# Kernel tuning notes

Hardware: AMD Instinct MI355X
Metric: run time of the kernel (lower is better)

Reference implementation:

```python
import jax, jax.numpy as jnp
import numpy as np

# ROIAlign config (torchvision semantics, aligned=False)
SPATIAL_SCALE = 0.25
POOLED = 7
SAMPLING_RATIO = 2
MODE = "max"  # from __init__ mode='max'


def setup_inputs() -> dict:
    key = jax.random.key(0)
    kf, kcx, kcy, kw, kh, kb = jax.random.split(key, 6)
    B, C, H, W = 2, 256, 200, 304
    N = 512
    IMG_H, IMG_W = H / SPATIAL_SCALE, W / SPATIAL_SCALE
    feature = jax.random.normal(kf, (B, C, H, W), dtype=jnp.float32)
    cx = jax.random.uniform(kcx, (N,)) * IMG_W
    cy = jax.random.uniform(kcy, (N,)) * IMG_H
    bw = jax.random.uniform(kw, (N,)) * 192.0 + 16.0
    bh = jax.random.uniform(kh, (N,)) * 192.0 + 16.0
    x1 = jnp.clip(cx - bw * 0.5, 0.0, IMG_W - 2.0)
    y1 = jnp.clip(cy - bh * 0.5, 0.0, IMG_H - 2.0)
    x2 = jnp.clip(cx + bw * 0.5, x1 + 1.0, IMG_W - 1.0)
    y2 = jnp.clip(cy + bh * 0.5, y1 + 1.0, IMG_H - 1.0)
    boxes = jnp.stack([x1, y1, x2, y2], axis=1).astype(jnp.float32)
    batch_idx = jax.random.randint(kb, (N,), 0, B, dtype=jnp.int32)
    return {"feature": feature, "boxes": boxes, "batch_idx": batch_idx}


def _sample_coords(start, size):
    # start,size: [N]; returns [N, POOLED*SAMPLING_RATIO] sample coordinates
    bin_sz = size / POOLED                         # [N]
    p = jnp.arange(POOLED, dtype=jnp.float32)      # bin index
    s = (jnp.arange(SAMPLING_RATIO, dtype=jnp.float32) + 0.5) / SAMPLING_RATIO
    # coord = start + (p + s) * bin_sz  -> [N, POOLED, RATIO]
    c = start[:, None, None] + (p[None, :, None] + s[None, None, :]) * bin_sz[:, None, None]
    return c.reshape(c.shape[0], POOLED * SAMPLING_RATIO)


def roi_align(feature, boxes, batch_idx):
    B, C, H, W = feature.shape
    roi = boxes * SPATIAL_SCALE                    # [N,4] in feature coords
    rs_x, rs_y, re_x, re_y = roi[:, 0], roi[:, 1], roi[:, 2], roi[:, 3]
    roi_w = jnp.maximum(re_x - rs_x, 1.0)
    roi_h = jnp.maximum(re_y - rs_y, 1.0)
    ys = _sample_coords(rs_y, roi_h)               # [N, Sy]
    xs = _sample_coords(rs_x, roi_w)               # [N, Sx]
    y = jnp.broadcast_to(ys[:, :, None], (ys.shape[0], ys.shape[1], xs.shape[1]))
    x = jnp.broadcast_to(xs[:, None, :], y.shape)  # [N, Sy, Sx]

    valid = (y > -1.0) & (y < H) & (x > -1.0) & (x < W)
    y = jnp.clip(y, 0.0, H - 1)
    x = jnp.clip(x, 0.0, W - 1)
    y0 = jnp.floor(y).astype(jnp.int32)
    x0 = jnp.floor(x).astype(jnp.int32)
    y1 = jnp.minimum(y0 + 1, H - 1)
    x1 = jnp.minimum(x0 + 1, W - 1)
    ly = y - y0.astype(y.dtype)
    lx = x - x0.astype(x.dtype)
    hy, hx = 1.0 - ly, 1.0 - lx
    b = batch_idx[:, None, None]
    # advanced indexing -> [N, Sy, Sx, C]
    val = (hy * hx)[..., None] * feature[b, :, y0, x0] \
        + (hy * lx)[..., None] * feature[b, :, y0, x1] \
        + (ly * hx)[..., None] * feature[b, :, y1, x0] \
        + (ly * lx)[..., None] * feature[b, :, y1, x1]
    val = jnp.where(valid[..., None], val, 0.0)
    N = boxes.shape[0]
    val = val.reshape(N, POOLED, SAMPLING_RATIO, POOLED, SAMPLING_RATIO, C)
    if MODE == "max":
        out = val.max(axis=(2, 4))                 # [N, PH, PW, C]
    else:
        out = val.mean(axis=(2, 4))
    return jnp.transpose(out, (0, 3, 1, 2))        # [N, C, PH, PW]


def reference(feature, boxes, batch_idx):
    return roi_align(feature, boxes, batch_idx)
```

## Files before the change

### kernel.cpp

```cpp
#include <hip/hip_runtime.h>


#define SS 0.25f
#define POOLED 7

constexpr int Cc = 256;
constexpr int Hc = 200;
constexpr int Wc = 304;
constexpr int Nc = 512;

constexpr int CELLS   = 49;
constexpr int PER_BOX = Cc * CELLS;
constexpr int PLANE   = Hc * Wc;
constexpr int NSAMP   = 14;
constexpr int TILES   = Cc / 4;
constexpr int DEPTH   = 5;
constexpr int GRPF    = 260;
constexpr int BUF_A   = 4 * GRPF;
constexpr int BUF_B   = 3 * GRPF;
constexpr int WAVE_A  = DEPTH * BUF_A;
constexpr int WAVE_B  = DEPTH * BUF_B;
constexpr int CH_F    = WAVE_A + WAVE_B;
constexpr int LDS_F   = 4 * CH_F;
constexpr size_t WS_NEED = (size_t)Nc * sizeof(int);

__global__ __launch_bounds__(64) void box_rank_kernel(
    const float* __restrict__ boxes,
    const int*   __restrict__ batch_idx,
    int*         __restrict__ perm)
{
    const int n = blockIdx.x;
    const int l = threadIdx.x;

    const float cyn  = (boxes[n * 4 + 1] + boxes[n * 4 + 3]) * (0.5f * SS);
    const int  bandn = min(3, max(0, (int)(cyn * (4.0f / (float)Hc))));
    const int  keyn  = batch_idx[n] * 4 + bandn;

    int rank = 0;
    #pragma unroll
    for (int m = 0; m < Nc / 64; ++m) {
        const int j = m * 64 + l;
        const float cyj  = (boxes[j * 4 + 1] + boxes[j * 4 + 3]) * (0.5f * SS);
        const int  bandj = min(3, max(0, (int)(cyj * (4.0f / (float)Hc))));
        const int  keyj  = batch_idx[j] * 4 + bandj;
        const bool lt = (keyj < keyn) || (keyj == keyn && j < n);
        rank += (int)__popcll(__ballot(lt));
    }
    if (l == 0) perm[rank] = n;
}

template <bool USE_PERM>
__global__ __launch_bounds__(512) void roi_align_max_kernel(
    const float* __restrict__ feature,
    const float* __restrict__ boxes,
    const int*   __restrict__ batch_idx,
    const int*   __restrict__ perm,
    float*       __restrict__ out)
{
    __shared__ float lds[LDS_F];

    const int bid = blockIdx.x;
    const int n = USE_PERM ? perm[(bid & 7) * 64 + (bid >> 3)] : bid;
    const int tid  = threadIdx.x;
    const int wv   = tid >> 6;
    const int lane = tid & 63;
    const int chl  = wv >> 1;
    const int role = wv & 1;
    const int NI    = role ? 3 : 4;
    const int BUF   = role ? BUF_B : BUF_A;
    const int wbase = chl * CH_F + (role ? WAVE_A : 0);
    const int HALF  = role ? 6 : 8;
    const int SYB   = role ? 8 : 0;
    const int NCELL = role ? 21 : 28;
    const int lane16 = lane & 15;
    const int rquad  = lane >> 4;

    const float rsx = boxes[n * 4 + 0] * SS;
    const float rsy = boxes[n * 4 + 1] * SS;
    const float rex = boxes[n * 4 + 2] * SS;
    const float rey = boxes[n * 4 + 3] * SS;
    const float roi_w = fmaxf(rex - rsx, 1.0f);
    const float roi_h = fmaxf(rey - rsy, 1.0f);
    const float bin_w = roi_w / (float)POOLED;
    const float bin_h = roi_h / (float)POOLED;
    const int   b     = batch_idx[n];

    const float x_first = __fadd_rn(rsx, __fmul_rn(0.25f, bin_w));
    const float xc0     = fminf(fmaxf(x_first, 0.0f), (float)(Wc - 1));
    const int   xbase   = ((int)floorf(xc0)) & ~3;

    const float x_last = __fadd_rn(rsx, __fmul_rn(6.75f, bin_w));
    const float xlc    = fminf(fmaxf(x_last, 0.0f), (float)(Wc - 1));
    const int   x0l    = (int)floorf(xlc);
    const int   xlastc = min(x0l + 1, Wc - 1);
    const int   span   = xlastc - xbase + 1;
    const int   nl4    = (span + 4) >> 2;

    int ro[4];
    #pragma unroll
    for (int i = 0; i < 4; ++i) {
        const int ls    = i * 4 + rquad;
        const int which = ls >= HALF;
        const int sY    = SYB + (which ? ls - HALF : ls);
        const float py  = fmaf((float)sY, 0.5f, 0.25f);
        const float fy  = __fadd_rn(rsy, __fmul_rn(py, bin_h));
        const float fyc = fminf(fmaxf(fy, 0.0f), (float)(Hc - 1));
        const int   y0  = (int)floorf(fyc);
        ro[i] = (which ? min(y0 + 1, Hc - 1) : y0) * Wc;
    }
    const int  col = min(xbase + lane16 * 4, Wc - 4);
    const bool act = (lane16 < nl4);

    const int cidx = min(lane, NCELL - 1);
    const int ph   = (role ? 4 : 0) + cidx / 7;
    const int pw   = cidx % 7;

    float w00[2][2], w01[2][2], w10[2][2], w11[2][2];
    int   a0t[2][2], a1t[2][2];
    #pragma unroll
    for (int sy = 0; sy < 2; ++sy) {
        const int   sY  = ph * 2 + sy;
        const float py  = (float)ph + ((float)sy + 0.5f) * 0.5f;
        const float fy  = __fadd_rn(rsy, __fmul_rn(py, bin_h));
        const bool  vy  = (fy > -1.0f) && (fy < (float)Hc);
        const float fyc = fminf(fmaxf(fy, 0.0f), (float)(Hc - 1));
        const int   y0i = (int)floorf(fyc);
        const float ly  = fyc - (float)y0i;
        const float hy  = 1.0f - ly;
        #pragma unroll
        for (int sx = 0; sx < 2; ++sx) {
            const float px  = (float)pw + ((float)sx + 0.5f) * 0.5f;
            const float fx  = __fadd_rn(rsx, __fmul_rn(px, bin_w));
            const bool  vx  = (fx > -1.0f) && (fx < (float)Wc);
            const float fxc = fminf(fmaxf(fx, 0.0f), (float)(Wc - 1));
            const int   x0i = (int)floorf(fxc);
            const float lx  = fxc - (float)x0i;
            const float hx  = 1.0f - lx;
            const int   c0  = x0i - xbase;
            const bool  v   = vy && vx;
            w00[sy][sx] = v ? hy * hx : 0.0f;
            w01[sy][sx] = v ? hy * lx : 0.0f;
            w10[sy][sx] = v ? ly * hx : 0.0f;
            w11[sy][sx] = v ? ly * lx : 0.0f;
            const int lsY = sY - SYB;
            const int ls0 = lsY;
            const int ls1 = lsY + HALF;
            a0t[sy][sx] = (ls0 >> 2) * GRPF + (ls0 & 3) * 64 + c0;
            a1t[sy][sx] = (ls1 >> 2) * GRPF + (ls1 & 3) * 64 + c0;
        }
    }

#define ISSUE(PTR, QOFF)                                                      \
    if (act) {                                                                \
        for (int i = 0; i < NI; ++i) {                                        \
            const float* gsrc = (PTR) + ro[i] + col;                          \
            const int lofs = __builtin_amdgcn_readfirstlane(                  \
                (wbase + (QOFF) + i * GRPF) * 4);                             \
            __builtin_amdgcn_global_load_lds(                                 \
                (const __attribute__((address_space(1))) unsigned int*)       \
                    (const void*)gsrc,                                        \
                (__attribute__((address_space(3))) unsigned int*)             \
                    (void*)((char*)lds + lofs),                               \
                16, 0, 0);                                                    \
        }                                                                     \
    }

    const float* gp0 = feature + ((size_t)b * Cc + chl) * (size_t)PLANE;
    {
        const float* gpt = gp0;
        #pragma unroll
        for (int tt = 0; tt < 4; ++tt) {
            ISSUE(gpt, tt * BUF)
            gpt += (size_t)4 * PLANE;
        }
    }
    const float* gIss = gp0 + (size_t)16 * PLANE;
    int qI = 4 * BUF;
    int qC = 0;
    const int QMAX = DEPTH * BUF;
    float* outp = out + (size_t)n * PER_BOX + chl * CELLS
                + (role ? 28 : 0) + cidx;

    for (int t = 0; t < TILES; ++t) {
        if (t < TILES - 4) {
            ISSUE(gIss, qI)
            gIss += (size_t)4 * PLANE;
            qI += BUF; if (qI == QMAX) qI = 0;
            if (role == 0) asm volatile("s_waitcnt vmcnt(16)" ::: "memory");
            else           asm volatile("s_waitcnt vmcnt(12)" ::: "memory");
        } else {
            asm volatile("s_waitcnt vmcnt(0)" ::: "memory");
        }

        const int qb = wbase + qC;
        float m = -INFINITY;
        #pragma unroll
        for (int sy = 0; sy < 2; ++sy) {
            #pragma unroll
            for (int sx = 0; sx < 2; ++sx) {
                const int a0 = qb + a0t[sy][sx];
                const int a1 = qb + a1t[sy][sx];
                const float bil = w00[sy][sx] * lds[a0]
                                + w01[sy][sx] * lds[a0 + 1]
                                + w10[sy][sx] * lds[a1]
                                + w11[sy][sx] * lds[a1 + 1];
                m = fmaxf(m, bil);
            }
        }
        if (lane < NCELL) *outp = m;
        outp += 4 * CELLS;
        qC += BUF; if (qC == QMAX) qC = 0;
    }
#undef ISSUE
}

extern "C" void kernel_launch(void* const* d_in, const int* in_sizes, int n_in,
                              void* d_out, int out_size, void* d_ws, size_t ws_size,
                              hipStream_t stream) {
    const float* feature   = (const float*)d_in[0];
    const float* boxes     = (const float*)d_in[1];
    const int*   batch_idx = (const int*)d_in[2];
    float*       out       = (float*)d_out;

    if (d_ws != nullptr && ws_size >= WS_NEED) {
        int* perm = (int*)d_ws;
        box_rank_kernel<<<Nc, 64, 0, stream>>>(boxes, batch_idx, perm);
        roi_align_max_kernel<true><<<Nc, 512, 0, stream>>>(
            feature, boxes, batch_idx, perm, out);
    } else {
        roi_align_max_kernel<false><<<Nc, 512, 0, stream>>>(
            feature, boxes, batch_idx, nullptr, out);
    }
}
```

Before: 246.8 us.

## Split each box across two 256-thread blocks with double-buffered LDS pipeline

Each ROI is now handled by two blocks, each covering 128 channels, so the grid doubles and the block shrinks from 512 to 256 threads. The 5-deep per-wave LDS ring becomes a 2-stage double buffer, with vmcnt waits retuned to match. This cuts the LDS footprint per block sharply, so several blocks can be resident per CU and latency is hidden by more concurrent waves instead of deep in-block prefetch. The trade-off is less prefetch depth inside each wave and per-box setup work (coordinate and weight computation) done twice.

After: 235.7 us. 4.5% less time.

```diff
diff --git a/kernel.cpp b/kernel.cpp
--- a/kernel.cpp
+++ b/kernel.cpp
@@ -12,16 +12,12 @@
 constexpr int CELLS   = 49;
 constexpr int PER_BOX = Cc * CELLS;
 constexpr int PLANE   = Hc * Wc;
-constexpr int NSAMP   = 14;
-constexpr int TILES   = Cc / 4;
-constexpr int DEPTH   = 5;
+constexpr int TILES   = 64;
 constexpr int GRPF    = 260;
 constexpr int BUF_A   = 4 * GRPF;
 constexpr int BUF_B   = 3 * GRPF;
-constexpr int WAVE_A  = DEPTH * BUF_A;
-constexpr int WAVE_B  = DEPTH * BUF_B;
-constexpr int CH_F    = WAVE_A + WAVE_B;
-constexpr int LDS_F   = 4 * CH_F;
+constexpr int CH_F    = 2 * (BUF_A + BUF_B);
+constexpr int LDS_F   = 2 * CH_F;
 constexpr size_t WS_NEED = (size_t)Nc * sizeof(int);
 
 __global__ __launch_bounds__(64) void box_rank_kernel(
@@ -50,7 +46,7 @@
 }
 
 template <bool USE_PERM>
-__global__ __launch_bounds__(512) void roi_align_max_kernel(
+__global__ __launch_bounds__(256) void roi_align_max_kernel(
     const float* __restrict__ feature,
     const float* __restrict__ boxes,
     const int*   __restrict__ batch_idx,
@@ -59,8 +55,10 @@
 {
     __shared__ float lds[LDS_F];
 
-    const int bid = blockIdx.x;
-    const int n = USE_PERM ? perm[(bid & 7) * 64 + (bid >> 3)] : bid;
+    const int bid  = blockIdx.x;
+    const int half = bid >> 9;
+    const int i0   = bid & 511;
+    const int n    = USE_PERM ? perm[(i0 & 7) * 64 + (i0 >> 3)] : i0;
     const int tid  = threadIdx.x;
     const int wv   = tid >> 6;
     const int lane = tid & 63;
@@ -68,7 +66,7 @@
     const int role = wv & 1;
     const int NI    = role ? 3 : 4;
     const int BUF   = role ? BUF_B : BUF_A;
-    const int wbase = chl * CH_F + (role ? WAVE_A : 0);
+    const int wbase = chl * CH_F + (role ? 2 * BUF_A : 0);
     const int HALF  = role ? 6 : 8;
     const int SYB   = role ? 8 : 0;
     const int NCELL = role ? 21 : 28;
@@ -165,53 +163,56 @@
         }                                                                     \
     }
 
-    const float* gp0 = feature + ((size_t)b * Cc + chl) * (size_t)PLANE;
-    {
-        const float* gpt = gp0;
-        #pragma unroll
-        for (int tt = 0; tt < 4; ++tt) {
-            ISSUE(gpt, tt * BUF)
-            gpt += (size_t)4 * PLANE;
-        }
-    }
-    const float* gIss = gp0 + (size_t)16 * PLANE;
-    int qI = 4 * BUF;
-    int qC = 0;
-    const int QMAX = DEPTH * BUF;
-    float* outp = out + (size_t)n * PER_BOX + chl * CELLS
+#define COMPUTE(QSEL)                                                         \
+    {                                                                         \
+        const int qb = wbase + (QSEL) * BUF;                                  \
+        float m = -INFINITY;                                                  \
+        _Pragma("unroll")                                                     \
+        for (int sy = 0; sy < 2; ++sy) {                                      \
+            _Pragma("unroll")                                                 \
+            for (int sx = 0; sx < 2; ++sx) {                                  \
+                const int a0 = qb + a0t[sy][sx];                              \
+                const int a1 = qb + a1t[sy][sx];                              \
+                const float bil = w00[sy][sx] * lds[a0]                       \
+                                + w01[sy][sx] * lds[a0 + 1]                   \
+                                + w10[sy][sx] * lds[a1]                       \
+                                + w11[sy][sx] * lds[a1 + 1];                  \
+                m = fmaxf(m, bil);                                            \
+            }                                                                 \
+        }                                                                     \
+        if (lane < NCELL) *outp = m;                                          \
+        outp += 2 * CELLS;                                                    \
+    }
+
+    const float* gp = feature
+        + ((size_t)b * Cc + 128 * half + chl) * (size_t)PLANE;
+    float* outp = out + (size_t)n * PER_BOX
+                + (size_t)(128 * half + chl) * CELLS
                 + (role ? 28 : 0) + cidx;
 
-    for (int t = 0; t < TILES; ++t) {
-        if (t < TILES - 4) {
-            ISSUE(gIss, qI)
-            gIss += (size_t)4 * PLANE;
-            qI += BUF; if (qI == QMAX) qI = 0;
-            if (role == 0) asm volatile("s_waitcnt vmcnt(16)" ::: "memory");
-            else           asm volatile("s_waitcnt vmcnt(12)" ::: "memory");
-        } else {
-            asm volatile("s_waitcnt vmcnt(0)" ::: "memory");
-        }
-
-        const int qb = wbase + qC;
-        float m = -INFINITY;
-        #pragma unroll
-        for (int sy = 0; sy < 2; ++sy) {
-            #pragma unroll
-            for (int sx = 0; sx < 2; ++sx) {
-                const int a0 = qb + a0t[sy][sx];
-                const int a1 = qb + a1t[sy][sx];
-                const float bil = w00[sy][sx] * lds[a0]
-                                + w01[sy][sx] * lds[a0 + 1]
-                                + w10[sy][sx] * lds[a1]
-                                + w11[sy][sx] * lds[a1 + 1];
-                m = fmaxf(m, bil);
-            }
-        }
-        if (lane < NCELL) *outp = m;
-        outp += 4 * CELLS;
-        qC += BUF; if (qC == QMAX) qC = 0;
-    }
+    asm volatile("s_waitcnt vmcnt(0)" ::: "memory");
+
+    ISSUE(gp, 0)
+    gp += (size_t)2 * PLANE;
+
+    ISSUE(gp, BUF)
+    gp += (size_t)2 * PLANE;
+    if (role == 0) asm volatile("s_waitcnt vmcnt(4)" ::: "memory");
+    else           asm volatile("s_waitcnt vmcnt(3)" ::: "memory");
+    COMPUTE(0)
+
+    for (int t = 1; t <= TILES - 2; ++t) {
+        ISSUE(gp, ((t + 1) & 1) * BUF)
+        gp += (size_t)2 * PLANE;
+        if (role == 0) asm volatile("s_waitcnt vmcnt(5)" ::: "memory");
+        else           asm volatile("s_waitcnt vmcnt(4)" ::: "memory");
+        COMPUTE(t & 1)
+    }
+
+    asm volatile("s_waitcnt vmcnt(1)" ::: "memory");
+    COMPUTE((TILES - 1) & 1)
 #undef ISSUE
+#undef COMPUTE
 }
 
 extern "C" void kernel_launch(void* const* d_in, const int* in_sizes, int n_in,
@@ -222,13 +223,14 @@
     const int*   batch_idx = (const int*)d_in[2];
     float*       out       = (float*)d_out;
 
+    const int grid = 2 * Nc;
     if (d_ws != nullptr && ws_size >= WS_NEED) {
         int* perm = (int*)d_ws;
         box_rank_kernel<<<Nc, 64, 0, stream>>>(boxes, batch_idx, perm);
-        roi_align_max_kernel<true><<<Nc, 512, 0, stream>>>(
+        roi_align_max_kernel<true><<<grid, 256, 0, stream>>>(
             feature, boxes, batch_idx, perm, out);
     } else {
-        roi_align_max_kernel<false><<<Nc, 512, 0, stream>>>(
+        roi_align_max_kernel<false><<<grid, 256, 0, stream>>>(
             feature, boxes, batch_idx, nullptr, out);
     }
 }
```
